# Kernel tuning notes

Measured on AMD Instinct MI355X. Metric: run time of the kernel, lower is better.

## Reference

```python
import jax
jax.config.update("jax_enable_x64", True)  # codes use *1e12 factors; need int64
import jax.numpy as jnp
import numpy as np

# HashRectsPt hyperparameters (module buffers)
W0, H0 = 512.0, 512.0
ALPHA = 1.2
GAMMA = 0.6
BX, BY = 0.5, 0.5
N_RECTS = 8192


def setup_inputs() -> dict:
    key = jax.random.key(0)
    k1, k2, k3 = jax.random.split(key, 3)
    xy = jax.random.uniform(k1, (N_RECTS, 2), minval=0.0, maxval=2000.0)
    wh = jax.random.uniform(k2, (N_RECTS, 2), minval=8.0, maxval=512.0)
    rects = jnp.concatenate([xy, wh], axis=1).astype(jnp.float32)  # [N,4] x,y,w,h
    conf = jax.random.uniform(k3, (N_RECTS,), dtype=jnp.float32)
    return {"rects": rects, "conf": conf}


def _hash_codes(rects):
    # HashRectsPt.__call__ -> packed single int64 code per rect
    x, y, w, h = rects[:, 0], rects[:, 1], rects[:, 2], rects[:, 3]
    log_alpha = jnp.log(jnp.float32(ALPHA))
    i = jnp.round((jnp.log(jnp.float32(W0)) - jnp.log(w)) / log_alpha)
    j = jnp.round((jnp.log(jnp.float32(H0)) - jnp.log(h)) / log_alpha)
    gamma_ratio = (1.0 - GAMMA) / (1.0 + GAMMA)
    di = (W0 * gamma_ratio) / (ALPHA ** i)
    dj = (H0 * gamma_ratio) / (ALPHA ** j)
    # b_is_relative=True branch
    qx = jnp.round(x / di - BX)
    qy = jnp.round(y / dj - BY)
    codes = (qx.astype(jnp.int64)
             + qy.astype(jnp.int64) * 10_000
             + i.astype(jnp.int64) * 100_000_000
             + j.astype(jnp.int64) * 1_000_000_000_000)
    return codes  # [N] int64


def reference(rects, conf):
    codes = _hash_codes(rects)                         # [N]
    n = codes.shape[0]
    # torch.unique with data-dependent U -> padded fixed-size unique (U<=N);
    # pad value can never equal a real code, so padded columns match nothing.
    uniq = jnp.unique(codes, size=n, fill_value=jnp.iinfo(jnp.int64).min)  # [N]
    assign = codes[:, None] == uniq[None, :]           # [N, U] bool
    scores = conf[:, None] * assign.astype(conf.dtype)  # [N, U]
    # torch .max(dim=0) returns first max index; jnp.argmax matches.
    argidx = jnp.argmax(scores, axis=0)                # [U]
    return argidx
```

## Files before the change

### kernel.cpp

```cpp
#include <hip/hip_runtime.h>
#include <hip/hip_bf16.h>
#include <math.h>

#define N 8192
#define S 32
#define SLICE (N / S)
#define IBLK 256

__device__ __forceinline__ long long hash_code(float x, float y, float w, float h) {
    const float LOG_ALPHA = (float)log((double)1.2f);
    const float LOGW0     = (float)log(512.0);
    float i_f = rintf((LOGW0 - (float)log((double)w)) / LOG_ALPHA);
    float j_f = rintf((LOGW0 - (float)log((double)h)) / LOG_ALPHA);
    float pi  = (float)pow((double)1.2f, (double)i_f);
    float pj  = (float)pow((double)1.2f, (double)j_f);
    float qx  = rintf(x / (128.0f / pi) - 0.5f);
    float qy  = rintf(y / (128.0f / pj) - 0.5f);
    return (long long)qx
         + (long long)qy * 10000LL
         + (long long)i_f * 100000000LL
         + (long long)j_f * 1000000000000LL;
}

__global__ void k_codes(const float4* __restrict__ rects,
                        const float* __restrict__ conf,
                        ulonglong2* __restrict__ pair,
                        int* __restrict__ lose,
                        int* __restrict__ rank,
                        int* __restrict__ out) {
    int t = blockIdx.x * blockDim.x + threadIdx.x;
    float4 r = rects[t];
    unsigned long long code = (unsigned long long)hash_code(r.x, r.y, r.z, r.w);
    unsigned long long key  = ((unsigned long long)__float_as_uint(conf[t]) << 32)
                            | (unsigned int)(N - 1 - t);
    pair[t] = make_ulonglong2(code, key);
    lose[t] = 0;
    rank[t] = 0;
    out[t]  = 0;
}

__global__ void __launch_bounds__(IBLK)
k_winner(const ulonglong2* __restrict__ pair, int* __restrict__ lose) {
    __shared__ ulonglong2 s_p[SLICE];
    int t = threadIdx.x;
    int i = blockIdx.x * IBLK + t;
    s_p[t] = pair[blockIdx.y * SLICE + t];
    ulonglong2 me = pair[i];
    __syncthreads();
    int l = 0;
    #pragma unroll 8
    for (int k = 0; k < SLICE; ++k) {
        ulonglong2 p = s_p[k];
        l |= (int)((p.x == me.x) & (p.y > me.y));
    }
    if (l) atomicOr(&lose[i], 1);
}

__global__ void __launch_bounds__(IBLK)
k_rank(const ulonglong2* __restrict__ pair, const int* __restrict__ lose,
       int* __restrict__ rank) {
    __shared__ unsigned long long s_cw[SLICE];
    int t = threadIdx.x;
    int i = blockIdx.x * IBLK + t;
    int jb = blockIdx.y * SLICE + t;
    s_cw[t] = (pair[jb].x << 1) | (unsigned long long)(lose[jb] == 0);
    unsigned long long ci2 = pair[i].x << 1;
    __syncthreads();
    int r = 0;
    #pragma unroll 8
    for (int k = 0; k < SLICE; ++k) {
        unsigned long long cw = s_cw[k];
        r += (int)(cw & 1ULL) & (int)(cw < ci2);
    }
    if (r) atomicAdd(&rank[i], r);
}

__global__ void k_scatter(const float* __restrict__ conf,
                          const int* __restrict__ lose,
                          const int* __restrict__ rank,
                          int* __restrict__ out) {
    int i = blockIdx.x * blockDim.x + threadIdx.x;
    if (lose[i] == 0) {
        out[rank[i]] = (conf[i] == 0.0f) ? 0 : i;
    }
}

extern "C" void kernel_launch(void* const* d_in, const int* in_sizes, int n_in,
                              void* d_out, int out_size, void* d_ws, size_t ws_size,
                              hipStream_t stream) {
    const float4* rects = (const float4*)d_in[0];
    const float*  conf  = (const float*)d_in[1];
    int* out = (int*)d_out;

    char* ws = (char*)d_ws;
    ulonglong2* pair = (ulonglong2*)ws;
    int* lose = (int*)(ws + N * sizeof(ulonglong2));
    int* rank = (int*)(ws + N * sizeof(ulonglong2) + N * 4);

    k_codes  <<<N / 256, 256, 0, stream>>>(rects, conf, pair, lose, rank, out);
    k_winner <<<dim3(N / IBLK, S), IBLK, 0, stream>>>(pair, lose);
    k_rank   <<<dim3(N / IBLK, S), IBLK, 0, stream>>>(pair, lose, rank);
    k_scatter<<<N / 256, 256, 0, stream>>>(conf, lose, rank, out);
}
```

Baseline: 77.72 us.

## Pack hash codes into 32 bits and replace rank atomics with partial sums

The 64-bit decimal hash code becomes a 32-bit bit-packed code. The winner key is now a single 64-bit word holding the code and the confidence, with ties broken by index. The shared-memory staging in the winner and rank kernels is replaced by direct uniform global loads, and the rank atomics are replaced by per-slice partial counts that the scatter kernel sums. This halves the comparison width, removes the atomics and the rank zeroing, and keeps the same ordering only if the packed fields stay within their bit ranges and qx/qy are non-negative. The bit packing assumes bounded ranges for i, j, qx and qy, which may not hold for every input, and out-of-range values would change the unique ordering.

```diff
diff --git a/kernel.cpp b/kernel.cpp
--- a/kernel.cpp
+++ b/kernel.cpp
@@ -7,7 +7,7 @@
 #define SLICE (N / S)
 #define IBLK 256
 
-__device__ __forceinline__ long long hash_code(float x, float y, float w, float h) {
+__device__ __forceinline__ unsigned pack_code(float x, float y, float w, float h) {
     const float LOG_ALPHA = (float)log((double)1.2f);
     const float LOGW0     = (float)log(512.0);
     float i_f = rintf((LOGW0 - (float)log((double)w)) / LOG_ALPHA);
@@ -16,72 +16,69 @@
     float pj  = (float)pow((double)1.2f, (double)j_f);
     float qx  = rintf(x / (128.0f / pi) - 0.5f);
     float qy  = rintf(y / (128.0f / pj) - 0.5f);
-    return (long long)qx
-         + (long long)qy * 10000LL
-         + (long long)i_f * 100000000LL
-         + (long long)j_f * 1000000000000LL;
+    return ((unsigned)(int)j_f << 27) | ((unsigned)(int)i_f << 22)
+         | ((unsigned)(int)qy << 11) | (unsigned)(int)qx;
 }
 
 __global__ void k_codes(const float4* __restrict__ rects,
                         const float* __restrict__ conf,
-                        ulonglong2* __restrict__ pair,
+                        unsigned* __restrict__ code32,
+                        unsigned long long* __restrict__ pairw,
                         int* __restrict__ lose,
-                        int* __restrict__ rank,
                         int* __restrict__ out) {
     int t = blockIdx.x * blockDim.x + threadIdx.x;
     float4 r = rects[t];
-    unsigned long long code = (unsigned long long)hash_code(r.x, r.y, r.z, r.w);
-    unsigned long long key  = ((unsigned long long)__float_as_uint(conf[t]) << 32)
-                            | (unsigned int)(N - 1 - t);
-    pair[t] = make_ulonglong2(code, key);
+    unsigned c = pack_code(r.x, r.y, r.z, r.w);
+    code32[t] = c;
+    pairw[t]  = ((unsigned long long)c << 32) | (unsigned long long)__float_as_uint(conf[t]);
     lose[t] = 0;
-    rank[t] = 0;
     out[t]  = 0;
 }
 
 __global__ void __launch_bounds__(IBLK)
-k_winner(const ulonglong2* __restrict__ pair, int* __restrict__ lose) {
-    __shared__ ulonglong2 s_p[SLICE];
-    int t = threadIdx.x;
-    int i = blockIdx.x * IBLK + t;
-    s_p[t] = pair[blockIdx.y * SLICE + t];
-    ulonglong2 me = pair[i];
-    __syncthreads();
+k_winner(const unsigned long long* __restrict__ pairw, int* __restrict__ lose) {
+    int i = blockIdx.x * IBLK + threadIdx.x;
+    int jbase = blockIdx.y * SLICE;
+    unsigned long long wi = pairw[i];
+    unsigned wi_hi = (unsigned)(wi >> 32);
     int l = 0;
-    #pragma unroll 8
+    #pragma unroll 16
     for (int k = 0; k < SLICE; ++k) {
-        ulonglong2 p = s_p[k];
-        l |= (int)((p.x == me.x) & (p.y > me.y));
+        unsigned long long wj = pairw[jbase + k];
+        bool same = (unsigned)(wj >> 32) == wi_hi;
+        bool beat = same && ((wj > wi) || ((wj == wi) && (jbase + k < i)));
+        l |= (int)beat;
     }
     if (l) atomicOr(&lose[i], 1);
 }
 
 __global__ void __launch_bounds__(IBLK)
-k_rank(const ulonglong2* __restrict__ pair, const int* __restrict__ lose,
-       int* __restrict__ rank) {
-    __shared__ unsigned long long s_cw[SLICE];
-    int t = threadIdx.x;
-    int i = blockIdx.x * IBLK + t;
-    int jb = blockIdx.y * SLICE + t;
-    s_cw[t] = (pair[jb].x << 1) | (unsigned long long)(lose[jb] == 0);
-    unsigned long long ci2 = pair[i].x << 1;
-    __syncthreads();
+k_rank(const unsigned* __restrict__ code32, const int* __restrict__ lose,
+       int* __restrict__ rank_part) {
+    int i = blockIdx.x * IBLK + threadIdx.x;
+    int jbase = blockIdx.y * SLICE;
+    unsigned ci = code32[i];
     int r = 0;
-    #pragma unroll 8
+    #pragma unroll 16
     for (int k = 0; k < SLICE; ++k) {
-        unsigned long long cw = s_cw[k];
-        r += (int)(cw & 1ULL) & (int)(cw < ci2);
+        unsigned cj = code32[jbase + k];
+        int lj = lose[jbase + k];
+        unsigned val = lj ? 0xFFFFFFFFu : cj;
+        r += (int)(val < ci);
     }
-    if (r) atomicAdd(&rank[i], r);
+    rank_part[blockIdx.y * N + i] = r;
 }
 
 __global__ void k_scatter(const float* __restrict__ conf,
                           const int* __restrict__ lose,
-                          const int* __restrict__ rank,
+                          const int* __restrict__ rank_part,
                           int* __restrict__ out) {
     int i = blockIdx.x * blockDim.x + threadIdx.x;
+    int r = 0;
+    #pragma unroll
+    for (int s = 0; s < S; ++s) r += rank_part[s * N + i];
     if (lose[i] == 0) {
-        out[rank[i]] = (conf[i] == 0.0f) ? 0 : i;
+        out[r] = (conf[i] == 0.0f) ? 0 : i;
     }
 }
 
@@ -93,12 +90,13 @@
     int* out = (int*)d_out;
 
     char* ws = (char*)d_ws;
-    ulonglong2* pair = (ulonglong2*)ws;
-    int* lose = (int*)(ws + N * sizeof(ulonglong2));
-    int* rank = (int*)(ws + N * sizeof(ulonglong2) + N * 4);
+    unsigned long long* pairw = (unsigned long long*)ws;
+    unsigned* code32 = (unsigned*)(ws + N * 8);
+    int*      lose   = (int*)(ws + N * 8 + N * 4);
+    int*      rank_part = (int*)(ws + N * 8 + N * 4 + N * 4);
 
-    k_codes  <<<N / 256, 256, 0, stream>>>(rects, conf, pair, lose, rank, out);
-    k_winner <<<dim3(N / IBLK, S), IBLK, 0, stream>>>(pair, lose);
-    k_rank   <<<dim3(N / IBLK, S), IBLK, 0, stream>>>(pair, lose, rank);
-    k_scatter<<<N / 256, 256, 0, stream>>>(conf, lose, rank, out);
+    k_codes  <<<N / 256, 256, 0, stream>>>(rects, conf, code32, pairw, lose, out);
+    k_winner <<<dim3(N / IBLK, S), IBLK, 0, stream>>>(pairw, lose);
+    k_rank   <<<dim3(N / IBLK, S), IBLK, 0, stream>>>(code32, lose, rank_part);
+    k_scatter<<<N / 256, 256, 0, stream>>>(conf, lose, rank_part, out);
 }
```

Measured after the change: 94.44 us. 1.22x slower.
